# Optimization experiments

Measured on AMD Instinct MI355X. Metric: run time of the kernel, lower is better.

Reference implementation:

```python
import jax, jax.numpy as jnp
import numpy as np

NUM_NODES = 50000
NUM_EDGES = 800000
NUM_GRAPHS = 512
NUM_LAYERS = 4
BN_EPS = 1e-5


def batchnorm(z, gamma, beta):
    mu = jnp.mean(z, axis=0)
    var = jnp.mean((z - mu) ** 2, axis=0)  # biased, as torch BN training forward
    return (z - mu) * jax.lax.rsqrt(var + BN_EPS) * gamma + beta


def setup_inputs() -> dict:
    key = jax.random.key(0)
    ks = jax.random.split(key, 16)
    inp = {
        "x": jax.random.randint(ks[0], (NUM_NODES,), 0, 32),
        "edge_index": jax.random.randint(ks[1], (2, NUM_EDGES), 0, NUM_NODES),
        "batch": jnp.sort(jax.random.randint(ks[2], (NUM_NODES,), 0, NUM_GRAPHS)),
        "emb": jax.random.normal(ks[3], (32, 64), jnp.float32) * 0.1,
        "W1": jax.random.normal(ks[4], (NUM_LAYERS, 64, 128), jnp.float32) * 0.1,
        "b1": jax.random.normal(ks[5], (NUM_LAYERS, 128), jnp.float32) * 0.1,
        "g1": jax.random.uniform(ks[6], (NUM_LAYERS, 128), jnp.float32, 0.5, 1.5),
        "bt1": jax.random.normal(ks[7], (NUM_LAYERS, 128), jnp.float32) * 0.1,
        "W2": jax.random.normal(ks[8], (NUM_LAYERS, 128, 64), jnp.float32) * 0.1,
        "b2": jax.random.normal(ks[9], (NUM_LAYERS, 64), jnp.float32) * 0.1,
        "gbn": jax.random.uniform(ks[10], (NUM_LAYERS - 1, 64), jnp.float32, 0.5, 1.5),
        "bbn": jax.random.normal(ks[11], (NUM_LAYERS - 1, 64), jnp.float32) * 0.1,
        "Wh1": jax.random.normal(ks[12], (64, 32), jnp.float32) * 0.1,
        "bh1": jax.random.normal(ks[13], (32,), jnp.float32) * 0.1,
        "Wh2": jax.random.normal(ks[14], (32, 10), jnp.float32) * 0.1,
        "bh2": jax.random.normal(ks[15], (10,), jnp.float32) * 0.1,
    }
    return inp


def reference(x, edge_index, batch, emb, W1, b1, g1, bt1, W2, b2, gbn, bbn, Wh1, bh1, Wh2, bh2):
    n = x.shape[0]
    src, dst = edge_index[0], edge_index[1]
    h = emb[x]  # [N, 64]
    eps = 0.0
    for i in range(NUM_LAYERS):
        agg = jax.ops.segment_sum(h[src], dst, num_segments=n)  # scatter-add neighbors
        z = (1.0 + eps) * h + agg
        z = jax.nn.relu(batchnorm(z @ W1[i] + b1[i], g1[i], bt1[i]))
        h = jax.nn.relu(z @ W2[i] + b2[i])  # GINConv output + outer ReLU
        if i < NUM_LAYERS - 1:
            h = batchnorm(h, gbn[i], bbn[i])
    g = jax.ops.segment_sum(h, batch, num_segments=NUM_GRAPHS)  # global_add_pool
    out = jax.nn.relu(g @ Wh1 + bh1) @ Wh2 + bh2  # dropout is identity (eval)
    return out
```

## Files before the change

### kernel.cpp

```cpp
#include <hip/hip_runtime.h>

#define NN 50000
#define NE 800000
#define NG 512
#define TPB 256
#define BN_EPS 1e-5f
#define NBLK_G 784
#define EDGE_BLKS 3125
#define EMB_BLKS 6250
#define HIST_BLKS 128
#define HIST_EPB 6250
#define HIST_WORDS 12500
#define TPB_FIN 1024

typedef __attribute__((ext_vector_type(8))) short bf16x8;
typedef __attribute__((ext_vector_type(4))) float f32x4;

__device__ __forceinline__ float bf2f(unsigned u) {
  return __uint_as_float(u << 16);
}
__device__ __forceinline__ unsigned f2bf(float f) {
  unsigned u = __float_as_uint(f);
  u += 0x7FFFu + ((u >> 16) & 1u);
  return u >> 16;
}

__global__ __launch_bounds__(TPB) void k_hist_lds(const int* __restrict__ dst,
                                                  unsigned* __restrict__ partial,
                                                  unsigned char* __restrict__ rank8) {
  __shared__ unsigned hist[HIST_WORDS];
  const int t = threadIdx.x, b = blockIdx.x;
  for (int w = t; w < HIST_WORDS; w += TPB) hist[w] = 0u;
  __syncthreads();
  const int* dp = dst + b * HIST_EPB;
  unsigned char* rp = rank8 + b * HIST_EPB;
  for (int it = t; it < HIST_EPB; it += TPB) {
    int d = dp[it];
    unsigned sh = 8u * (d & 3);
    unsigned old = atomicAdd(&hist[d >> 2], 1u << sh);
    rp[it] = (unsigned char)((old >> sh) & 255u);
  }
  __syncthreads();
  unsigned* out = partial + (size_t)b * HIST_WORDS;
  for (int w = t; w < HIST_WORDS; w += TPB) out[w] = hist[w];
}

__global__ void k_hist_scan(unsigned* __restrict__ partial, int* __restrict__ counts) {
  int w = blockIdx.x * TPB + threadIdx.x;
  if (w >= HIST_WORDS) return;
  unsigned run = 0;
#pragma unroll 8
  for (int b = 0; b < HIST_BLKS; ++b) {
    unsigned v = partial[(size_t)b * HIST_WORDS + w];
    partial[(size_t)b * HIST_WORDS + w] = run;
    run += v;
  }
  *(int4*)&counts[4 * w] = make_int4((int)(run & 255u), (int)((run >> 8) & 255u),
                                     (int)((run >> 16) & 255u), (int)(run >> 24));
}

__global__ void k_scan1(const int* __restrict__ counts, int* __restrict__ incl,
                        int* __restrict__ btot) {
  __shared__ int lds[TPB];
  int i = blockIdx.x * TPB + threadIdx.x;
  int v = (i < NN) ? counts[i] : 0;
  lds[threadIdx.x] = v;
  __syncthreads();
  for (int off = 1; off < TPB; off <<= 1) {
    int t = (threadIdx.x >= off) ? lds[threadIdx.x - off] : 0;
    __syncthreads();
    lds[threadIdx.x] += t;
    __syncthreads();
  }
  if (i < NN) incl[i] = lds[threadIdx.x];
  if (threadIdx.x == TPB - 1) btot[blockIdx.x] = lds[TPB - 1];
}

__global__ void k_scan23(const int* __restrict__ incl, const int* __restrict__ btot,
                         int* __restrict__ row_ptr) {
  __shared__ int lds[TPB];
  const int t = threadIdx.x, b = blockIdx.x;
  lds[t] = (t < 196 && t < b) ? btot[t] : 0;
  __syncthreads();
  for (int off = TPB / 2; off > 0; off >>= 1) {
    if (t < off) lds[t] += lds[t + off];
    __syncthreads();
  }
  int S = lds[0];
  int i = b * TPB + t;
  if (i == 0) row_ptr[0] = 0;
  if (i < NN) row_ptr[i + 1] = incl[i] + S;
}

__global__ __launch_bounds__(TPB) void k_fill_embed(
    const int* __restrict__ src, const int* __restrict__ dst,
    const unsigned* __restrict__ partial, const unsigned char* __restrict__ rank8,
    const int* __restrict__ row_ptr, unsigned short* __restrict__ srcs,
    const int* __restrict__ x, const float* __restrict__ emb,
    unsigned* __restrict__ h_bf) {
  int b = blockIdx.x;
  if (b < EDGE_BLKS) {
    int e = b * TPB + threadIdx.x;
    int d = dst[e];
    int bh = e / HIST_EPB;
    unsigned base = (partial[(size_t)bh * HIST_WORDS + (d >> 2)] >> (8u * (d & 3))) & 255u;
    int pos = row_ptr[d] + (int)base + (int)rank8[e];
    srcs[pos] = (unsigned short)src[e];
  } else {
    int i = (b - EDGE_BLKS) * TPB + threadIdx.x;
    int n = i >> 5, l = i & 31;
    float2 ev = *(const float2*)&emb[x[n] * 64 + 2 * l];
    h_bf[i] = f2bf(ev.x) | (f2bf(ev.y) << 16);
  }
}

template <bool BN>
__global__ void k_aggregate_bf(const unsigned* __restrict__ h_bf,
                               const int* __restrict__ row_ptr,
                               const unsigned short* __restrict__ srcs,
                               const float* __restrict__ bnst,
                               unsigned* __restrict__ zb) {
  int wid = (blockIdx.x * TPB + threadIdx.x) >> 6;
  int lane = threadIdx.x & 63;
  if (wid >= NN) return;
  int half = lane >> 5, l = lane & 31;
  int beg = row_ptr[wid], end = row_ptr[wid + 1];
  float a0 = 0.f, a1 = 0.f;
  if (half == 0) {
    unsigned u = h_bf[(size_t)wid * 32 + l];
    a0 = bf2f(u & 0xFFFF);
    a1 = bf2f(u >> 16);
  }
  for (int e = beg + half; e < end; e += 16) {
    int idx[8];
#pragma unroll
    for (int k = 0; k < 8; ++k) {
      int ee = e + 2 * k;
      idx[k] = srcs[ee < end ? ee : end - 1];
    }
    unsigned uu[8];
#pragma unroll
    for (int k = 0; k < 8; ++k) uu[k] = h_bf[(size_t)idx[k] * 32 + l];
#pragma unroll
    for (int k = 0; k < 8; ++k) {
      bool v = (e + 2 * k) < end;
      a0 += v ? bf2f(uu[k] & 0xFFFF) : 0.f;
      a1 += v ? bf2f(uu[k] >> 16) : 0.f;
    }
  }
  a0 += __shfl_xor(a0, 32);
  a1 += __shfl_xor(a1, 32);
  if (half == 0) {
    float zv0, zv1;
    if constexpr (BN) {
      float2 scv = *(const float2*)&bnst[2 * l];
      float2 shv = *(const float2*)&bnst[64 + 2 * l];
      float d1 = (float)(1 + end - beg);
      zv0 = fmaf(scv.x, a0, d1 * shv.x);
      zv1 = fmaf(scv.y, a1, d1 * shv.y);
    } else {
      zv0 = a0;
      zv1 = a1;
    }
    zb[(size_t)wid * 32 + l] = f2bf(zv0) | (f2bf(zv1) << 16);
  }
}

__global__ __launch_bounds__(TPB) void k_gemm1(const unsigned short* __restrict__ zb,
                                               const float* __restrict__ W,
                                               const float* __restrict__ bias,
                                               unsigned short* __restrict__ z2b,
                                               float* __restrict__ partials) {
  __shared__ __align__(16) unsigned short WTl[128 * 72];
  const int t = threadIdx.x;
  const int r0 = blockIdx.x * 64;
#pragma unroll
  for (int it = 0; it < 8192 / TPB; ++it) {
    int idx = t + it * TPB;
    WTl[(idx & 127) * 72 + (idx >> 7)] = (unsigned short)f2bf(W[idx]);
  }
  __syncthreads();

  const int w = t >> 6, lane = t & 63;
  const int m16 = lane & 15, kg = lane >> 4;
  const int ra = r0 + w * 16 + m16;
  bf16x8 a0 = {0, 0, 0, 0, 0, 0, 0, 0}, a1 = {0, 0, 0, 0, 0, 0, 0, 0};
  if (ra < NN) {
    a0 = *(const bf16x8*)&zb[(size_t)ra * 64 + kg * 8];
    a1 = *(const bf16x8*)&zb[(size_t)ra * 64 + 32 + kg * 8];
  }
  f32x4 acc[8];
#pragma unroll
  for (int f = 0; f < 8; ++f) acc[f] = f32x4{0.f, 0.f, 0.f, 0.f};
#pragma unroll
  for (int f = 0; f < 8; ++f) {
    bf16x8 b0 = *(const bf16x8*)&WTl[(f * 16 + m16) * 72 + kg * 8];
    bf16x8 b1 = *(const bf16x8*)&WTl[(f * 16 + m16) * 72 + 32 + kg * 8];
    acc[f] = __builtin_amdgcn_mfma_f32_16x16x32_bf16(a0, b0, acc[f], 0, 0, 0);
    acc[f] = __builtin_amdgcn_mfma_f32_16x16x32_bf16(a1, b1, acc[f], 0, 0, 0);
  }
  __syncthreads();
  float* Ss = (float*)WTl;
  float* Sq = Ss + 512;
  const int rwb = r0 + w * 16 + kg * 4;
#pragma unroll
  for (int f = 0; f < 8; ++f) {
    int col = f * 16 + m16;
    float bc = bias[col];
    float cs = 0.f, cq = 0.f;
#pragma unroll
    for (int j = 0; j < 4; ++j) {
      int rw = rwb + j;
      if (rw < NN) {
        float v = acc[f][j] + bc;
        z2b[(size_t)rw * 128 + col] = (unsigned short)f2bf(v);
        cs += v;
        cq += v * v;
      }
    }
    cs += __shfl_xor(cs, 16); cs += __shfl_xor(cs, 32);
    cq += __shfl_xor(cq, 16); cq += __shfl_xor(cq, 32);
    if (kg == 0) {
      Ss[w * 128 + col] = cs;
      Sq[w * 128 + col] = cq;
    }
  }
  __syncthreads();
  if (t < 128) {
    float ss = Ss[t] + Ss[128 + t] + Ss[256 + t] + Ss[384 + t];
    float qq = Sq[t] + Sq[128 + t] + Sq[256 + t] + Sq[384 + t];
    partials[blockIdx.x * 256 + t] = ss;
    partials[blockIdx.x * 256 + 128 + t] = qq;
  }
}

template <bool STATS>
__global__ __launch_bounds__(TPB) void k_gemm2(const unsigned short* __restrict__ z2b,
                                               const float* __restrict__ W,
                                               const float* __restrict__ bias,
                                               const float* __restrict__ bnst,
                                               unsigned short* __restrict__ outp,
                                               float* __restrict__ partials) {
  __shared__ __align__(16) unsigned short WTl[64 * 136];
  __shared__ float scl[128], shl[128];
  const int t = threadIdx.x;
  const int r0 = blockIdx.x * 64;
#pragma unroll
  for (int it = 0; it < 8192 / TPB; ++it) {
    int idx = t + it * TPB;
    WTl[(idx & 63) * 136 + (idx >> 6)] = (unsigned short)f2bf(W[idx]);
  }
  if (t < 128) {
    scl[t] = bnst[t];
    shl[t] = bnst[128 + t];
  }
  __syncthreads();

  const int w = t >> 6, lane = t & 63;
  const int m16 = lane & 15, kg = lane >> 4;
  const int ra = r0 + w * 16 + m16;
  f32x4 acc[4];
#pragma unroll
  for (int f = 0; f < 4; ++f) acc[f] = f32x4{0.f, 0.f, 0.f, 0.f};
#pragma unroll
  for (int s = 0; s < 4; ++s) {
    int k0 = s * 32 + kg * 8;
    bf16x8 a = {0, 0, 0, 0, 0, 0, 0, 0};
    if (ra < NN) {
      bf16x8 raw = *(const bf16x8*)&z2b[(size_t)ra * 128 + k0];
#pragma unroll
      for (int i = 0; i < 8; ++i) {
        float v = bf2f((unsigned)(unsigned short)raw[i]);
        v = fmaxf(fmaf(v, scl[k0 + i], shl[k0 + i]), 0.f);
        a[i] = (short)f2bf(v);
      }
    }
#pragma unroll
    for (int f = 0; f < 4; ++f) {
      bf16x8 b = *(const bf16x8*)&WTl[(f * 16 + m16) * 136 + k0];
      acc[f] = __builtin_amdgcn_mfma_f32_16x16x32_bf16(a, b, acc[f], 0, 0, 0);
    }
  }
  __syncthreads();
  float* Ss = (float*)WTl;
  float* Sq = Ss + 256;
  const int rwb = r0 + w * 16 + kg * 4;
#pragma unroll
  for (int f = 0; f < 4; ++f) {
    int col = f * 16 + m16;
    float bc = bias[col];
    float cs = 0.f, cq = 0.f;
#pragma unroll
    for (int j = 0; j < 4; ++j) {
      int rw = rwb + j;
      if (rw < NN) {
        float v = fmaxf(acc[f][j] + bc, 0.f);
        outp[(size_t)rw * 64 + col] = (unsigned short)f2bf(v);
        if constexpr (STATS) {
          cs += v;
          cq += v * v;
        }
      }
    }
    if constexpr (STATS) {
      cs += __shfl_xor(cs, 16); cs += __shfl_xor(cs, 32);
      cq += __shfl_xor(cq, 16); cq += __shfl_xor(cq, 32);
      if (kg == 0) {
        Ss[w * 64 + col] = cs;
        Sq[w * 64 + col] = cq;
      }
    }
  }
  if constexpr (STATS) {
    __syncthreads();
    if (t < 64) {
      float ss = Ss[t] + Ss[64 + t] + Ss[128 + t] + Ss[192 + t];
      float qq = Sq[t] + Sq[64 + t] + Sq[128 + t] + Sq[192 + t];
      partials[blockIdx.x * 128 + t] = ss;
      partials[blockIdx.x * 128 + 64 + t] = qq;
    }
  }
}

template <int C>
__global__ __launch_bounds__(TPB_FIN) void k_finalize(const float* __restrict__ partials,
                                                      const float* __restrict__ gamma,
                                                      const float* __restrict__ beta,
                                                      float* __restrict__ out) {
  constexpr int G = TPB_FIN / C;
  constexpr int IT = NBLK_G / G;
  __shared__ float lds[2 * TPB_FIN];
  const int c = threadIdx.x % C, g = threadIdx.x / C;
  const float* p = partials + g * 2 * C + c;
  float s = 0.f, s2 = 0.f;
#pragma unroll 8
  for (int bb = 0; bb < IT; ++bb) {
    s += p[(size_t)bb * G * 2 * C];
    s2 += p[(size_t)bb * G * 2 * C + C];
  }
  lds[threadIdx.x] = s;
  lds[TPB_FIN + threadIdx.x] = s2;
  __syncthreads();
  if (g == 0) {
#pragma unroll
    for (int k = 1; k < G; ++k) {
      s += lds[k * C + c];
      s2 += lds[TPB_FIN + k * C + c];
    }
    float invN = 1.0f / NN;
    float mu = s * invN;
    float var = s2 * invN - mu * mu;
    float rs = rsqrtf(var + BN_EPS) * gamma[c];
    out[c] = rs;
    out[C + c] = beta[c] - mu * rs;
  }
}

__global__ void k_poolhead(const unsigned* __restrict__ h_bf,
                           const int* __restrict__ batch,
                           const float* __restrict__ Wh1, const float* __restrict__ bh1,
                           const float* __restrict__ Wh2, const float* __restrict__ bh2,
                           float* __restrict__ out) {
  __shared__ float lds[2 * TPB];
  __shared__ float gl[64];
  __shared__ float hidl[32];
  int gi = blockIdx.x;
  int col = threadIdx.x & 31, grp = threadIdx.x >> 5;
  int a = 0, b = NN;
  while (a < b) { int m = (a + b) >> 1; if (batch[m] < gi) a = m + 1; else b = m; }
  int lo = a;
  b = NN;
  while (a < b) { int m = (a + b) >> 1; if (batch[m] < gi + 1) a = m + 1; else b = m; }
  int hi = a;
  float a0 = 0.f, a1 = 0.f;
  for (int n = lo + grp; n < hi; n += 8) {
    unsigned u = h_bf[(size_t)n * 32 + col];
    a0 += bf2f(u & 0xFFFF);
    a1 += bf2f(u >> 16);
  }
  lds[threadIdx.x] = a0;
  lds[TPB + threadIdx.x] = a1;
  __syncthreads();
  if (grp == 0) {
#pragma unroll
    for (int k = 1; k < 8; ++k) {
      a0 += lds[k * 32 + col];
      a1 += lds[TPB + k * 32 + col];
    }
    gl[2 * col] = a0;
    gl[2 * col + 1] = a1;
  }
  __syncthreads();
  if (threadIdx.x < 32) {
    int j = threadIdx.x;
    float hid = bh1[j];
    for (int k = 0; k < 64; ++k) hid = fmaf(gl[k], Wh1[k * 32 + j], hid);
    hidl[j] = fmaxf(hid, 0.f);
  }
  __syncthreads();
  if (threadIdx.x < 10) {
    int j = threadIdx.x;
    float o = bh2[j];
#pragma unroll
    for (int k = 0; k < 32; ++k) o = fmaf(hidl[k], Wh2[k * 10 + j], o);
    out[gi * 10 + j] = o;
  }
}

extern "C" void kernel_launch(void* const* d_in, const int* in_sizes, int n_in,
                              void* d_out, int out_size, void* d_ws, size_t ws_size,
                              hipStream_t stream) {
  const int* x = (const int*)d_in[0];
  const int* ei = (const int*)d_in[1];
  const int* batch = (const int*)d_in[2];
  const float* emb = (const float*)d_in[3];
  const float* W1 = (const float*)d_in[4];
  const float* b1 = (const float*)d_in[5];
  const float* g1 = (const float*)d_in[6];
  const float* bt1 = (const float*)d_in[7];
  const float* W2 = (const float*)d_in[8];
  const float* b2 = (const float*)d_in[9];
  const float* gbn = (const float*)d_in[10];
  const float* bbn = (const float*)d_in[11];
  const float* Wh1 = (const float*)d_in[12];
  const float* bh1 = (const float*)d_in[13];
  const float* Wh2 = (const float*)d_in[14];
  const float* bh2 = (const float*)d_in[15];
  float* out = (float*)d_out;

  const int* e_src = ei;
  const int* e_dst = ei + NE;

  char* ws = (char*)d_ws;
  size_t off = 0;
  auto alloc = [&](size_t bytes) -> void* {
    void* p = ws + off;
    off = (off + bytes + 255) & ~(size_t)255;
    return p;
  };
  unsigned* h_bf = (unsigned*)alloc((size_t)NN * 64 * 2);
  unsigned* zb = (unsigned*)alloc((size_t)NN * 64 * 2);
  unsigned short* z2b = (unsigned short*)alloc((size_t)NN * 128 * 2);
  unsigned short* srcs = (unsigned short*)alloc((size_t)NE * 2);
  unsigned char* rank8 = (unsigned char*)alloc((size_t)NE);
  int* row_ptr = (int*)alloc((size_t)(NN + 1) * 4);
  int* incl = (int*)alloc((size_t)NN * 4);
  int* btot = (int*)alloc(256 * 4);
  float* partials = (float*)alloc((size_t)NBLK_G * 256 * 4);
  float* statsL = (float*)alloc(4 * 256 * 4);
  float* statsH = (float*)alloc(3 * 128 * 4);
  int* counts = (int*)alloc((size_t)NN * 4);
  unsigned* histpart = (unsigned*)alloc((size_t)HIST_BLKS * HIST_WORDS * 4);

  k_hist_lds<<<HIST_BLKS, TPB, 0, stream>>>(e_dst, histpart, rank8);
  k_hist_scan<<<(HIST_WORDS + TPB - 1) / TPB, TPB, 0, stream>>>(histpart, counts);

  int nScanBlocks = (NN + TPB - 1) / TPB;
  k_scan1<<<nScanBlocks, TPB, 0, stream>>>(counts, incl, btot);
  k_scan23<<<nScanBlocks, TPB, 0, stream>>>(incl, btot, row_ptr);
  k_fill_embed<<<EDGE_BLKS + EMB_BLKS, TPB, 0, stream>>>(e_src, e_dst, histpart, rank8,
                                                         row_ptr, srcs, x, emb, h_bf);

  int gAgg = (NN * 64 + TPB - 1) / TPB;

  for (int i = 0; i < 4; ++i) {
    const float* W1i = W1 + (size_t)i * 64 * 128;
    const float* b1i = b1 + (size_t)i * 128;
    const float* g1i = g1 + (size_t)i * 128;
    const float* bt1i = bt1 + (size_t)i * 128;
    const float* W2i = W2 + (size_t)i * 128 * 64;
    const float* b2i = b2 + (size_t)i * 64;
    float* stL = statsL + (size_t)i * 256;

    if (i == 0)
      k_aggregate_bf<false><<<gAgg, TPB, 0, stream>>>(h_bf, row_ptr, srcs, nullptr, zb);
    else
      k_aggregate_bf<true><<<gAgg, TPB, 0, stream>>>(h_bf, row_ptr, srcs,
                                                     statsH + (size_t)(i - 1) * 128, zb);

    k_gemm1<<<NBLK_G, TPB, 0, stream>>>((const unsigned short*)zb, W1i, b1i, z2b, partials);
    k_finalize<128><<<1, TPB_FIN, 0, stream>>>(partials, g1i, bt1i, stL);

    if (i < 3) {
      float* stH = statsH + (size_t)i * 128;
      k_gemm2<true><<<NBLK_G, TPB, 0, stream>>>(z2b, W2i, b2i, stL,
                                                (unsigned short*)h_bf, partials);
      k_finalize<64><<<1, TPB_FIN, 0, stream>>>(partials, gbn + (size_t)i * 64,
                                                bbn + (size_t)i * 64, stH);
    } else {
      k_gemm2<false><<<NBLK_G, TPB, 0, stream>>>(z2b, W2i, b2i, stL,
                                                 (unsigned short*)h_bf, partials);
    }
  }

  k_poolhead<<<NG, TPB, 0, stream>>>(h_bf, batch, Wh1, bh1, Wh2, bh2, out);
}
```

Before: 308.1 us.

## Pre-convert GEMM weights to bf16 once and double rows per GEMM block

A new kernel converts all layer weights W1 and W2 to bf16 once at the start. The GEMM kernels now load those packed bf16 weights into LDS instead of converting fp32 weights in every block. Each GEMM block now covers 128 rows, two 16-row MFMA tiles per wave, so the LDS weight tile is reused across more rows and the grid shrinks from 784 to 400 blocks. The histogram pass also uses twice as many blocks with half the edges each. Fewer GEMM blocks means fewer resident waves per CU and more accumulator registers per thread, which could reduce latency hiding.

```diff
diff --git a/kernel.cpp b/kernel.cpp
--- a/kernel.cpp
+++ b/kernel.cpp
@@ -5,11 +5,11 @@
 #define NG 512
 #define TPB 256
 #define BN_EPS 1e-5f
-#define NBLK_G 784
+#define NBLK_G 400
 #define EDGE_BLKS 3125
 #define EMB_BLKS 6250
-#define HIST_BLKS 128
-#define HIST_EPB 6250
+#define HIST_BLKS 256
+#define HIST_EPB 3125
 #define HIST_WORDS 12500
 #define TPB_FIN 1024
 
@@ -23,6 +23,15 @@
   unsigned u = __float_as_uint(f);
   u += 0x7FFFu + ((u >> 16) & 1u);
   return u >> 16;
+}
+
+__global__ void k_wcvt(const float* __restrict__ W1, const float* __restrict__ W2,
+                       unsigned short* __restrict__ w1b, unsigned short* __restrict__ w2b) {
+  int i = blockIdx.x * TPB + threadIdx.x;
+  if (i < 32768)
+    w1b[i] = (unsigned short)f2bf(W1[i]);
+  else
+    w2b[i - 32768] = (unsigned short)f2bf(W2[i - 32768]);
 }
 
 __global__ __launch_bounds__(TPB) void k_hist_lds(const int* __restrict__ dst,
@@ -167,68 +176,89 @@
 }
 
 __global__ __launch_bounds__(TPB) void k_gemm1(const unsigned short* __restrict__ zb,
-                                               const float* __restrict__ W,
+                                               const unsigned short* __restrict__ w1b,
                                                const float* __restrict__ bias,
                                                unsigned short* __restrict__ z2b,
                                                float* __restrict__ partials) {
   __shared__ __align__(16) unsigned short WTl[128 * 72];
   const int t = threadIdx.x;
-  const int r0 = blockIdx.x * 64;
-#pragma unroll
-  for (int it = 0; it < 8192 / TPB; ++it) {
-    int idx = t + it * TPB;
-    WTl[(idx & 127) * 72 + (idx >> 7)] = (unsigned short)f2bf(W[idx]);
+  const int r0 = blockIdx.x * 128;
+#pragma unroll
+  for (int it = 0; it < 4096 / TPB; ++it) {
+    int i2 = t + it * TPB;
+    unsigned v = ((const unsigned*)w1b)[i2];
+    int idx = 2 * i2;
+    int k = idx >> 7, n = idx & 127;
+    WTl[n * 72 + k] = (unsigned short)(v & 0xFFFF);
+    WTl[(n + 1) * 72 + k] = (unsigned short)(v >> 16);
   }
   __syncthreads();
 
   const int w = t >> 6, lane = t & 63;
   const int m16 = lane & 15, kg = lane >> 4;
-  const int ra = r0 + w * 16 + m16;
-  bf16x8 a0 = {0, 0, 0, 0, 0, 0, 0, 0}, a1 = {0, 0, 0, 0, 0, 0, 0, 0};
-  if (ra < NN) {
-    a0 = *(const bf16x8*)&zb[(size_t)ra * 64 + kg * 8];
-    a1 = *(const bf16x8*)&zb[(size_t)ra * 64 + 32 + kg * 8];
-  }
-  f32x4 acc[8];
-#pragma unroll
-  for (int f = 0; f < 8; ++f) acc[f] = f32x4{0.f, 0.f, 0.f, 0.f};
+  bf16x8 a0[2], a1[2];
+#pragma unroll
+  for (int mi = 0; mi < 2; ++mi) {
+    int ra = r0 + w * 32 + mi * 16 + m16;
+    a0[mi] = bf16x8{0, 0, 0, 0, 0, 0, 0, 0};
+    a1[mi] = bf16x8{0, 0, 0, 0, 0, 0, 0, 0};
+    if (ra < NN) {
+      a0[mi] = *(const bf16x8*)&zb[(size_t)ra * 64 + kg * 8];
+      a1[mi] = *(const bf16x8*)&zb[(size_t)ra * 64 + 32 + kg * 8];
+    }
+  }
+  f32x4 acc[2][8];
+#pragma unroll
+  for (int mi = 0; mi < 2; ++mi)
+#pragma unroll
+    for (int f = 0; f < 8; ++f) acc[mi][f] = f32x4{0.f, 0.f, 0.f, 0.f};
 #pragma unroll
   for (int f = 0; f < 8; ++f) {
     bf16x8 b0 = *(const bf16x8*)&WTl[(f * 16 + m16) * 72 + kg * 8];
     bf16x8 b1 = *(const bf16x8*)&WTl[(f * 16 + m16) * 72 + 32 + kg * 8];
-    acc[f] = __builtin_amdgcn_mfma_f32_16x16x32_bf16(a0, b0, acc[f], 0, 0, 0);
-    acc[f] = __builtin_amdgcn_mfma_f32_16x16x32_bf16(a1, b1, acc[f], 0, 0, 0);
+#pragma unroll
+    for (int mi = 0; mi < 2; ++mi) {
+      acc[mi][f] = __builtin_amdgcn_mfma_f32_16x16x32_bf16(a0[mi], b0, acc[mi][f], 0, 0, 0);
+      acc[mi][f] = __builtin_amdgcn_mfma_f32_16x16x32_bf16(a1[mi], b1, acc[mi][f], 0, 0, 0);
+    }
   }
   __syncthreads();
   float* Ss = (float*)WTl;
-  float* Sq = Ss + 512;
-  const int rwb = r0 + w * 16 + kg * 4;
-#pragma unroll
-  for (int f = 0; f < 8; ++f) {
-    int col = f * 16 + m16;
-    float bc = bias[col];
-    float cs = 0.f, cq = 0.f;
-#pragma unroll
-    for (int j = 0; j < 4; ++j) {
-      int rw = rwb + j;
-      if (rw < NN) {
-        float v = acc[f][j] + bc;
-        z2b[(size_t)rw * 128 + col] = (unsigned short)f2bf(v);
-        cs += v;
-        cq += v * v;
+  float* Sq = Ss + 1024;
+#pragma unroll
+  for (int mi = 0; mi < 2; ++mi) {
+    const int rwb = r0 + w * 32 + mi * 16 + kg * 4;
+#pragma unroll
+    for (int f = 0; f < 8; ++f) {
+      int col = f * 16 + m16;
+      float bc = bias[col];
+      float cs = 0.f, cq = 0.f;
+#pragma unroll
+      for (int j = 0; j < 4; ++j) {
+        int rw = rwb + j;
+        if (rw < NN) {
+          float v = acc[mi][f][j] + bc;
+          z2b[(size_t)rw * 128 + col] = (unsigned short)f2bf(v);
+          cs += v;
+          cq += v * v;
+        }
       }
-    }
-    cs += __shfl_xor(cs, 16); cs += __shfl_xor(cs, 32);
-    cq += __shfl_xor(cq, 16); cq += __shfl_xor(cq, 32);
-    if (kg == 0) {
-      Ss[w * 128 + col] = cs;
-      Sq[w * 128 + col] = cq;
+      cs += __shfl_xor(cs, 16); cs += __shfl_xor(cs, 32);
+      cq += __shfl_xor(cq, 16); cq += __shfl_xor(cq, 32);
+      if (kg == 0) {
+        Ss[(w * 2 + mi) * 128 + col] = cs;
+        Sq[(w * 2 + mi) * 128 + col] = cq;
+      }
     }
   }
   __syncthreads();
   if (t < 128) {
-    float ss = Ss[t] + Ss[128 + t] + Ss[256 + t] + Ss[384 + t];
-    float qq = Sq[t] + Sq[128 + t] + Sq[256 + t] + Sq[384 + t];
+    float ss = 0.f, qq = 0.f;
+#pragma unroll
+    for (int g = 0; g < 8; ++g) {
+      ss += Ss[g * 128 + t];
+      qq += Sq[g * 128 + t];
+    }
     partials[blockIdx.x * 256 + t] = ss;
     partials[blockIdx.x * 256 + 128 + t] = qq;
   }
@@ -236,7 +266,7 @@
 
 template <bool STATS>
 __global__ __launch_bounds__(TPB) void k_gemm2(const unsigned short* __restrict__ z2b,
-                                               const float* __restrict__ W,
+                                               const unsigned short* __restrict__ w2b,
                                                const float* __restrict__ bias,
                                                const float* __restrict__ bnst,
                                                unsigned short* __restrict__ outp,
@@ -244,11 +274,15 @@
   __shared__ __align__(16) unsigned short WTl[64 * 136];
   __shared__ float scl[128], shl[128];
   const int t = threadIdx.x;
-  const int r0 = blockIdx.x * 64;
-#pragma unroll
-  for (int it = 0; it < 8192 / TPB; ++it) {
-    int idx = t + it * TPB;
-    WTl[(idx & 63) * 136 + (idx >> 6)] = (unsigned short)f2bf(W[idx]);
+  const int r0 = blockIdx.x * 128;
+#pragma unroll
+  for (int it = 0; it < 4096 / TPB; ++it) {
+    int i2 = t + it * TPB;
+    unsigned v = ((const unsigned*)w2b)[i2];
+    int idx = 2 * i2;
+    int k = idx >> 6, n = idx & 63;
+    WTl[n * 136 + k] = (unsigned short)(v & 0xFFFF);
+    WTl[(n + 1) * 136 + k] = (unsigned short)(v >> 16);
   }
   if (t < 128) {
     scl[t] = bnst[t];
@@ -258,64 +292,79 @@
 
   const int w = t >> 6, lane = t & 63;
   const int m16 = lane & 15, kg = lane >> 4;
-  const int ra = r0 + w * 16 + m16;
-  f32x4 acc[4];
-#pragma unroll
-  for (int f = 0; f < 4; ++f) acc[f] = f32x4{0.f, 0.f, 0.f, 0.f};
+  f32x4 acc[2][4];
+#pragma unroll
+  for (int mi = 0; mi < 2; ++mi)
+#pragma unroll
+    for (int f = 0; f < 4; ++f) acc[mi][f] = f32x4{0.f, 0.f, 0.f, 0.f};
 #pragma unroll
   for (int s = 0; s < 4; ++s) {
     int k0 = s * 32 + kg * 8;
-    bf16x8 a = {0, 0, 0, 0, 0, 0, 0, 0};
-    if (ra < NN) {
-      bf16x8 raw = *(const bf16x8*)&z2b[(size_t)ra * 128 + k0];
-#pragma unroll
-      for (int i = 0; i < 8; ++i) {
-        float v = bf2f((unsigned)(unsigned short)raw[i]);
-        v = fmaxf(fmaf(v, scl[k0 + i], shl[k0 + i]), 0.f);
-        a[i] = (short)f2bf(v);
+    bf16x8 a[2];
+#pragma unroll
+    for (int mi = 0; mi < 2; ++mi) {
+      int ra = r0 + w * 32 + mi * 16 + m16;
+      a[mi] = bf16x8{0, 0, 0, 0, 0, 0, 0, 0};
+      if (ra < NN) {
+        bf16x8 raw = *(const bf16x8*)&z2b[(size_t)ra * 128 + k0];
+#pragma unroll
+        for (int i = 0; i < 8; ++i) {
+          float v = bf2f((unsigned)(unsigned short)raw[i]);
+          v = fmaxf(fmaf(v, scl[k0 + i], shl[k0 + i]), 0.f);
+          a[mi][i] = (short)f2bf(v);
+        }
       }
     }
 #pragma unroll
     for (int f = 0; f < 4; ++f) {
       bf16x8 b = *(const bf16x8*)&WTl[(f * 16 + m16) * 136 + k0];
-      acc[f] = __builtin_amdgcn_mfma_f32_16x16x32_bf16(a, b, acc[f], 0, 0, 0);
+#pragma unroll
+      for (int mi = 0; mi < 2; ++mi)
+        acc[mi][f] = __builtin_amdgcn_mfma_f32_16x16x32_bf16(a[mi], b, acc[mi][f], 0, 0, 0);
     }
   }
   __syncthreads();
   float* Ss = (float*)WTl;
-  float* Sq = Ss + 256;
-  const int rwb = r0 + w * 16 + kg * 4;
-#pragma unroll
-  for (int f = 0; f < 4; ++f) {
-    int col = f * 16 + m16;
-    float bc = bias[col];
-    float cs = 0.f, cq = 0.f;
-#pragma unroll
-    for (int j = 0; j < 4; ++j) {
-      int rw = rwb + j;
-      if (rw < NN) {
-        float v = fmaxf(acc[f][j] + bc, 0.f);
-        outp[(size_t)rw * 64 + col] = (unsigned short)f2bf(v);
-        if constexpr (STATS) {
-          cs += v;
-          cq += v * v;
+  float* Sq = Ss + 512;
+#pragma unroll
+  for (int mi = 0; mi < 2; ++mi) {
+    const int rwb = r0 + w * 32 + mi * 16 + kg * 4;
+#pragma unroll
+    for (int f = 0; f < 4; ++f) {
+      int col = f * 16 + m16;
+      float bc = bias[col];
+      float cs = 0.f, cq = 0.f;
+#pragma unroll
+      for (int j = 0; j < 4; ++j) {
+        int rw = rwb + j;
+        if (rw < NN) {
+          float v = fmaxf(acc[mi][f][j] + bc, 0.f);
+          outp[(size_t)rw * 64 + col] = (unsigned short)f2bf(v);
+          if constexpr (STATS) {
+            cs += v;
+            cq += v * v;
+          }
         }
       }
-    }
-    if constexpr (STATS) {
-      cs += __shfl_xor(cs, 16); cs += __shfl_xor(cs, 32);
-      cq += __shfl_xor(cq, 16); cq += __shfl_xor(cq, 32);
-      if (kg == 0) {
-        Ss[w * 64 + col] = cs;
-        Sq[w * 64 + col] = cq;
+      if constexpr (STATS) {
+        cs += __shfl_xor(cs, 16); cs += __shfl_xor(cs, 32);
+        cq += __shfl_xor(cq, 16); cq += __shfl_xor(cq, 32);
+        if (kg == 0) {
+          Ss[(w * 2 + mi) * 64 + col] = cs;
+          Sq[(w * 2 + mi) * 64 + col] = cq;
+        }
       }
     }
   }
   if constexpr (STATS) {
     __syncthreads();
     if (t < 64) {
-      float ss = Ss[t] + Ss[64 + t] + Ss[128 + t] + Ss[192 + t];
-      float qq = Sq[t] + Sq[64 + t] + Sq[128 + t] + Sq[192 + t];
+      float ss = 0.f, qq = 0.f;
+#pragma unroll
+      for (int g = 0; g < 8; ++g) {
+        ss += Ss[g * 64 + t];
+        qq += Sq[g * 64 + t];
+      }
       partials[blockIdx.x * 128 + t] = ss;
       partials[blockIdx.x * 128 + 64 + t] = qq;
     }
@@ -451,7 +500,10 @@
   float* statsH = (float*)alloc(3 * 128 * 4);
   int* counts = (int*)alloc((size_t)NN * 4);
   unsigned* histpart = (unsigned*)alloc((size_t)HIST_BLKS * HIST_WORDS * 4);
-
+  unsigned short* w1b = (unsigned short*)alloc(32768 * 2);
+  unsigned short* w2b = (unsigned short*)alloc(32768 * 2);
+
+  k_wcvt<<<256, TPB, 0, stream>>>(W1, W2, w1b, w2b);
   k_hist_lds<<<HIST_BLKS, TPB, 0, stream>>>(e_dst, histpart, rank8);
   k_hist_scan<<<(HIST_WORDS + TPB - 1) / TPB, TPB, 0, stream>>>(histpart, counts);
 
@@ -464,11 +516,11 @@
   int gAgg = (NN * 64 + TPB - 1) / TPB;
 
   for (int i = 0; i < 4; ++i) {
-    const float* W1i = W1 + (size_t)i * 64 * 128;
+    const unsigned short* w1i = w1b + (size_t)i * 8192;
+    const unsigned short* w2i = w2b + (size_t)i * 8192;
     const float* b1i = b1 + (size_t)i * 128;
     const float* g1i = g1 + (size_t)i * 128;
     const float* bt1i = bt1 + (size_t)i * 128;
-    const float* W2i = W2 + (size_t)i * 128 * 64;
     const float* b2i = b2 + (size_t)i * 64;
     float* stL = statsL + (size_t)i * 256;
 
@@ -478,17 +530,17 @@
       k_aggregate_bf<true><<<gAgg, TPB, 0, stream>>>(h_bf, row_ptr, srcs,
                                                      statsH + (size_t)(i - 1) * 128, zb);
 
-    k_gemm1<<<NBLK_G, TPB, 0, stream>>>((const unsigned short*)zb, W1i, b1i, z2b, partials);
+    k_gemm1<<<NBLK_G, TPB, 0, stream>>>((const unsigned short*)zb, w1i, b1i, z2b, partials);
     k_finalize<128><<<1, TPB_FIN, 0, stream>>>(partials, g1i, bt1i, stL);
 
     if (i < 3) {
       float* stH = statsH + (size_t)i * 128;
-      k_gemm2<true><<<NBLK_G, TPB, 0, stream>>>(z2b, W2i, b2i, stL,
+      k_gemm2<true><<<NBLK_G, TPB, 0, stream>>>(z2b, w2i, b2i, stL,
                                                 (unsigned short*)h_bf, partials);
       k_finalize<64><<<1, TPB_FIN, 0, stream>>>(partials, gbn + (size_t)i * 64,
                                                 bbn + (size_t)i * 64, stH);
     } else {
-      k_gemm2<false><<<NBLK_G, TPB, 0, stream>>>(z2b, W2i, b2i, stL,
+      k_gemm2<false><<<NBLK_G, TPB, 0, stream>>>(z2b, w2i, b2i, stL,
                                                  (unsigned short*)h_bf, partials);
     }
   }
```

After: 307.7 us (median of 2 runs). About the same (-0.1%).
